# Kernel tuning notes

Measured on AMD Instinct MI355X. Metric: run time of the kernel, lower is better.

The kernel has to match this reference:

```python
import jax, jax.numpy as jnp
import numpy as np

B, D, K, H = 8192, 1024, 8, 2048


def setup_inputs() -> dict:
    key = jax.random.key(0)
    ks = jax.random.split(key, 4)
    x = jax.random.normal(ks[0], (B, D), dtype=jnp.float32)
    centroids = jax.random.normal(ks[1], (K, D), dtype=jnp.float32)
    W1 = jax.random.normal(ks[2], (K, D, H), dtype=jnp.float32) / np.sqrt(D).astype(np.float32)
    b1 = jnp.zeros((K, H), dtype=jnp.float32)
    W2 = jax.random.normal(ks[3], (K, H), dtype=jnp.float32) / np.sqrt(H).astype(np.float32)
    b2 = jnp.zeros((K,), dtype=jnp.float32)
    return {"x": x, "centroids": centroids, "W1": W1, "b1": b1, "W2": W2, "b2": b2}


def reference(x, centroids, W1, b1, W2, b2):
    # --- k-means hard routing: nearest centroid per sample (euclidean max_sim) ---
    # d2[b,k] = ||x_b||^2 - 2 x_b . c_k + ||c_k||^2  (avoid [B,K,D] blowup)
    d2 = (jnp.sum(x * x, axis=-1, keepdims=True)
          - 2.0 * (x @ centroids.T)
          + jnp.sum(centroids * centroids, axis=-1)[None, :])  # [B, K]
    cluster = jnp.argmin(d2, axis=-1)  # [B] int, hard assignment

    # --- per-expert log-likelihood heads (Einet stand-in), computed densely ---
    h = jnp.tanh(jnp.einsum("bd,kdh->kbh", x, W1) + b1[:, None, :])  # [K, B, H]
    lls = jnp.einsum("kbh,kh->kb", h, W2) + b2[:, None]              # [K, B]

    # --- combine: each sample takes the LL from its routed expert, original order ---
    lls_sorted = jnp.take_along_axis(lls.T, cluster[:, None], axis=1)[:, 0]  # [B]
    return lls_sorted
```

## Files before the change

kernel.cpp:

```cpp
#include <hip/hip_runtime.h>
#include <hip/hip_bf16.h>
#include <stdint.h>

#define B_N 8192
#define D_N 1024
#define K_N 8
#define H_N 2048

#define BM 320
#define BN 256
#define BK 64
#define GRID_MT 34
#define ABYTES 40960
#define BUFSZ 73728
#define RO_OFF 147456
#define PLL_OFF 148736
#define GEMM_LDS 153856

typedef unsigned int u32;
typedef unsigned short u16;
typedef __attribute__((ext_vector_type(8))) short short8;
typedef __attribute__((ext_vector_type(4))) float float4v;

struct __align__(8) us4 { u16 x, y, z, w; };

__device__ __forceinline__ u16 f2bf(float f) {
    union { float f; u32 u; } v; v.f = f;
    u32 u = v.u;
    u32 r = (u + 0x7fffu + ((u >> 16) & 1u)) >> 16;
    return (u16)r;
}

__device__ __forceinline__ float fast_tanh(float x) {
    float t = __expf(2.0f * x);
    return 1.0f - 2.0f * __builtin_amdgcn_rcpf(t + 1.0f);
}

__device__ __forceinline__ void async_copy16(void* lds, const void* g) {
    __builtin_amdgcn_global_load_lds(
        (const __attribute__((address_space(1))) void*)g,
        (__attribute__((address_space(3))) void*)lds, 16, 0, 0);
}

__global__ void route_kernel(const float* __restrict__ x,
                             const float* __restrict__ cent,
                             u16* __restrict__ xbf,
                             int* __restrict__ cluster,
                             u32* __restrict__ counts) {
    int tid = threadIdx.x;
    if (blockIdx.x == 0 && tid < K_N) counts[tid * 32] = 0;
    int wave = tid >> 6, lane = tid & 63;
    int b = blockIdx.x * 4 + wave;
    const float* xr = x + (size_t)b * D_N;

    float4 xv[4];
#pragma unroll
    for (int i = 0; i < 4; ++i)
        xv[i] = *(const float4*)(xr + i * 256 + lane * 4);

#pragma unroll
    for (int i = 0; i < 4; ++i) {
        us4 o;
        o.x = f2bf(xv[i].x); o.y = f2bf(xv[i].y);
        o.z = f2bf(xv[i].z); o.w = f2bf(xv[i].w);
        *(us4*)(xbf + (size_t)b * D_N + i * 256 + lane * 4) = o;
    }

    double acc[K_N];
#pragma unroll
    for (int k = 0; k < K_N; ++k) {
        const float* cr = cent + k * D_N;
        double s = 0.0;
#pragma unroll
        for (int i = 0; i < 4; ++i) {
            float4 cv = *(const float4*)(cr + i * 256 + lane * 4);
            double d0 = (double)xv[i].x - (double)cv.x; s += d0 * d0;
            double d1 = (double)xv[i].y - (double)cv.y; s += d1 * d1;
            double d2 = (double)xv[i].z - (double)cv.z; s += d2 * d2;
            double d3 = (double)xv[i].w - (double)cv.w; s += d3 * d3;
        }
        acc[k] = s;
    }
#pragma unroll
    for (int k = 0; k < K_N; ++k) {
        double v = acc[k];
        for (int off = 32; off; off >>= 1) v += __shfl_down(v, off);
        acc[k] = v;
    }
    if (lane == 0) {
        int best = 0; double bv = acc[0];
#pragma unroll
        for (int k = 1; k < K_N; ++k)
            if (acc[k] < bv) { bv = acc[k]; best = k; }
        cluster[b] = best;
    }
}

__global__ void scatter_kernel(const int* __restrict__ cluster,
                               u32* __restrict__ counts,
                               u32* __restrict__ idxl) {
    __shared__ u32 wcnt[4][K_N];
    __shared__ u32 gb[K_N];
    int tid = threadIdx.x;
    int b = blockIdx.x * 256 + tid;
    int lane = tid & 63, wid = tid >> 6;
    int cl = cluster[b];
    unsigned long long lower = (1ull << lane) - 1ull;
    u32 rank = 0;
#pragma unroll
    for (int k = 0; k < K_N; ++k) {
        unsigned long long mk = __ballot(cl == k);
        if (k == cl) rank = (u32)__popcll(mk & lower);
        if (lane == 0) wcnt[wid][k] = (u32)__popcll(mk);
    }
    __syncthreads();
    if (tid < K_N) {
        u32 tot = wcnt[0][tid] + wcnt[1][tid] + wcnt[2][tid] + wcnt[3][tid];
        gb[tid] = atomicAdd(&counts[tid * 32], tot);
    }
    __syncthreads();
    u32 woff = 0;
    if (wid > 0) woff += wcnt[0][cl];
    if (wid > 1) woff += wcnt[1][cl];
    if (wid > 2) woff += wcnt[2][cl];
    idxl[(size_t)cl * B_N + gb[cl] + woff + rank] = (u32)b;
}

__global__ void w1t_kernel(const float* __restrict__ w1, u16* __restrict__ w1t) {
    __shared__ float ts[64][65];
    int tid = threadIdx.x;
    int h0 = blockIdx.x * 64, d0 = blockIdx.y * 64, k = blockIdx.z;
    const float* src = w1 + ((size_t)k * D_N + d0) * H_N + h0;
#pragma unroll
    for (int i = 0; i < 4; ++i) {
        int q = i * 256 + tid;
        int r = q >> 4, c4 = (q & 15) * 4;
        float4 v = *(const float4*)(src + (size_t)r * H_N + c4);
        ts[c4 + 0][r] = v.x; ts[c4 + 1][r] = v.y;
        ts[c4 + 2][r] = v.z; ts[c4 + 3][r] = v.w;
    }
    __syncthreads();
    u16* dst = w1t + ((size_t)k * H_N + h0) * D_N + d0;
#pragma unroll
    for (int i = 0; i < 4; ++i) {
        int q = i * 256 + tid;
        int hr = q >> 4, d4 = (q & 15) * 4;
        us4 o;
        o.x = f2bf(ts[hr][d4 + 0]); o.y = f2bf(ts[hr][d4 + 1]);
        o.z = f2bf(ts[hr][d4 + 2]); o.w = f2bf(ts[hr][d4 + 3]);
        *(us4*)(dst + (size_t)hr * D_N + d4) = o;
    }
}

__global__ __launch_bounds__(512, 2) void gemm_kernel(
                            const u16* __restrict__ xbf,
                            const u16* __restrict__ w1t,
                            const float* __restrict__ b1,
                            const float* __restrict__ w2,
                            const u32* __restrict__ idxl,
                            const u32* __restrict__ counts,
                            float* __restrict__ llp) {
    extern __shared__ char lds[];
    int k = -1, mt = 0, ntile = 0;
#pragma unroll
    for (int kk = 0; kk < K_N; ++kk) {
        int c = (int)counts[kk * 32];
        int t = (c + BM - 1) / BM;
        if ((int)blockIdx.x >= ntile && (int)blockIdx.x < ntile + t) { k = kk; mt = (int)blockIdx.x - ntile; }
        ntile += t;
    }
    if (k < 0) return;
    int cnt = (int)counts[k * 32];
    int nc = blockIdx.y;
    int rows = cnt - mt * BM; if (rows > BM) rows = BM;
    int tid = threadIdx.x;
    int lane = tid & 63, w = tid >> 6;
    int wm = w >> 2, wn = w & 3;
    int wmbase = wm * 160;
    int h0 = nc * BN;
    int l15 = lane & 15, l4 = lane >> 4;

    u32* ro = (u32*)(lds + RO_OFF);
    float* pll = (float*)(lds + PLL_OFF);

    if (tid < BM) {
        int m = mt * BM + tid;
        int mm = m < cnt ? m : cnt - 1;
        ro[tid] = idxl[(size_t)k * B_N + mm] * (u32)(D_N * 2);
    }
    __syncthreads();

    u32 srcA[5], srcB[4];
#pragma unroll
    for (int i = 0; i < 5; ++i) {
        int c = i * 512 + tid; int r = c >> 3, j = c & 7;
        srcA[i] = ro[r] + ((u32)(j ^ (r & 7)) << 4);
    }
#pragma unroll
    for (int i = 0; i < 4; ++i) {
        int c = i * 512 + tid; int r = c >> 3, j = c & 7;
        srcB[i] = ((u32)(k * H_N + h0 + r) << 11) + ((u32)(j ^ (r & 7)) << 4);
    }
    const char* xb = (const char*)xbf;
    const char* wb = (const char*)w1t;

    int swz = l15 & 7;
    u32 aB0 = (u32)((wmbase + l15) * 128 + (((0 + l4) ^ swz) << 4));
    u32 aB1 = (u32)((wmbase + l15) * 128 + (((4 + l4) ^ swz) << 4));
    u32 bB0 = (u32)(ABYTES + (wn * 64 + l15) * 128 + (((0 + l4) ^ swz) << 4));
    u32 bB1 = (u32)(ABYTES + (wn * 64 + l15) * 128 + (((4 + l4) ^ swz) << 4));

    float4v acc[10][4];
#pragma unroll
    for (int mf = 0; mf < 10; ++mf)
#pragma unroll
        for (int nf = 0; nf < 4; ++nf)
            acc[mf][nf] = (float4v){0.f, 0.f, 0.f, 0.f};

#define STA(BUF, I, D) async_copy16((BUF) + (I) * 8192 + w * 1024, xb + srcA[I] + (D))
#define STB(BUF, I, D) async_copy16((BUF) + ABYTES + (I) * 8192 + w * 1024, wb + srcB[I] + (D))
#define BAR() do { asm volatile("" ::: "memory"); __builtin_amdgcn_s_barrier(); \
                   asm volatile("" ::: "memory"); } while (0)
#define LGKM0_PIN() do { asm volatile("s_waitcnt lgkmcnt(0)" ::: "memory"); \
                         __builtin_amdgcn_sched_barrier(0); } while (0)
#define MFMA_PHASE(MFB, BREG)                                                    \
    do {                                                                         \
        __builtin_amdgcn_s_setprio(1);                                           \
        _Pragma("unroll")                                                        \
        for (int i_ = 0; i_ < 5; ++i_) {                                         \
            if (wmbase + ((MFB) + i_) * 16 < rows) {                             \
                _Pragma("unroll")                                                \
                for (int nf_ = 0; nf_ < 4; ++nf_)                                \
                    acc[(MFB) + i_][nf_] = __builtin_amdgcn_mfma_f32_16x16x32_bf16( \
                        a[i_], BREG[nf_], acc[(MFB) + i_][nf_], 0, 0, 0);        \
            }                                                                    \
        }                                                                        \
        __builtin_amdgcn_s_setprio(0);                                           \
    } while (0)

    {
        char* Bp = lds;
        STA(Bp, 0, 0); STA(Bp, 1, 0); STA(Bp, 2, 0); STA(Bp, 3, 0); STA(Bp, 4, 0);
        STB(Bp, 0, 0); STB(Bp, 1, 0); STB(Bp, 2, 0); STB(Bp, 3, 0);
    }

    for (int t = 0; t < 16; ++t) {
        const char* Acur = lds + (t & 1) * BUFSZ;
        char* Bnx = lds + ((t + 1) & 1) * BUFSZ;
        u32 d = (u32)((t + 1) << 7);
        bool pre = (t < 15);
        short8 a[5], bC[4];

        asm volatile("s_waitcnt vmcnt(0)" ::: "memory");
        BAR();
#pragma unroll
        for (int nf = 0; nf < 4; ++nf)
            bC[nf] = *(const short8*)(Acur + bB0 + nf * 2048);
#pragma unroll
        for (int i = 0; i < 5; ++i)
            a[i] = *(const short8*)(Acur + aB0 + i * 2048);
        if (pre) { STB(Bnx, 0, d); STB(Bnx, 1, d); STB(Bnx, 2, d); }
        BAR();
        LGKM0_PIN();
        MFMA_PHASE(0, bC);

        BAR();
#pragma unroll
        for (int i = 0; i < 5; ++i)
            a[i] = *(const short8*)(Acur + aB0 + (5 + i) * 2048);
        if (pre) { STB(Bnx, 3, d); STA(Bnx, 0, d); STA(Bnx, 1, d); }
        BAR();
        LGKM0_PIN();
        MFMA_PHASE(5, bC);

        BAR();
#pragma unroll
        for (int nf = 0; nf < 4; ++nf)
            bC[nf] = *(const short8*)(Acur + bB1 + nf * 2048);
#pragma unroll
        for (int i = 0; i < 5; ++i)
            a[i] = *(const short8*)(Acur + aB1 + i * 2048);
        if (pre) { STA(Bnx, 2, d); STA(Bnx, 3, d); STA(Bnx, 4, d); }
        BAR();
        LGKM0_PIN();
        MFMA_PHASE(0, bC);

        BAR();
#pragma unroll
        for (int i = 0; i < 5; ++i)
            a[i] = *(const short8*)(Acur + aB1 + (5 + i) * 2048);
        BAR();
        LGKM0_PIN();
        MFMA_PHASE(5, bC);
    }

#undef STA
#undef STB
#undef BAR
#undef LGKM0_PIN
#undef MFMA_PHASE

    float w2v[4], b1v[4];
#pragma unroll
    for (int nf = 0; nf < 4; ++nf) {
        int h = h0 + wn * 64 + nf * 16 + l15;
        w2v[nf] = w2[k * H_N + h];
        b1v[nf] = b1[k * H_N + h];
    }
#pragma unroll
    for (int mf = 0; mf < 10; ++mf) {
        float rs[4] = {0.f, 0.f, 0.f, 0.f};
#pragma unroll
        for (int nf = 0; nf < 4; ++nf) {
#pragma unroll
            for (int r = 0; r < 4; ++r)
                rs[r] += fast_tanh(acc[mf][nf][r] + b1v[nf]) * w2v[nf];
        }
#pragma unroll
        for (int r = 0; r < 4; ++r) {
            float v = rs[r];
            v += __shfl_xor(v, 8);
            v += __shfl_xor(v, 4);
            v += __shfl_xor(v, 2);
            v += __shfl_xor(v, 1);
            if (l15 == 0) pll[wn * 320 + wmbase + mf * 16 + l4 * 4 + r] = v;
        }
    }
    __syncthreads();
    if (tid < BM) {
        int m = mt * BM + tid;
        if (m < cnt) {
            u32 b = idxl[(size_t)k * B_N + m];
            llp[(size_t)nc * B_N + b] = pll[tid] + pll[320 + tid] + pll[640 + tid] + pll[960 + tid];
        }
    }
}

__global__ void combine_kernel(const float* __restrict__ llp,
                               const int* __restrict__ cluster,
                               const float* __restrict__ b2,
                               float* __restrict__ out) {
    int b = blockIdx.x * 256 + threadIdx.x;
    float s = b2[cluster[b]];
#pragma unroll
    for (int nc = 0; nc < 8; ++nc) s += llp[(size_t)nc * B_N + b];
    out[b] = s;
}

extern "C" void kernel_launch(void* const* d_in, const int* in_sizes, int n_in,
                              void* d_out, int out_size, void* d_ws, size_t ws_size,
                              hipStream_t stream) {
    const float* x    = (const float*)d_in[0];
    const float* cent = (const float*)d_in[1];
    const float* W1   = (const float*)d_in[2];
    const float* b1   = (const float*)d_in[3];
    const float* W2   = (const float*)d_in[4];
    const float* b2   = (const float*)d_in[5];
    float* out = (float*)d_out;

    char* ws = (char*)d_ws;
    u16* xbf     = (u16*)(ws + 0);
    u16* w1t     = (u16*)(ws + 16777216);
    u32* counts  = (u32*)(ws + 50331648);
    int* cluster = (int*)(ws + 50332672);
    u32* idxl    = (u32*)(ws + 50365440);
    float* llp   = (float*)(ws + 50627584);

    (void)hipFuncSetAttribute((const void*)gemm_kernel,
                              hipFuncAttributeMaxDynamicSharedMemorySize, GEMM_LDS);

    hipLaunchKernelGGL(route_kernel, dim3(B_N / 4), dim3(256), 0, stream,
                       x, cent, xbf, cluster, counts);
    hipLaunchKernelGGL(scatter_kernel, dim3(32), dim3(256), 0, stream,
                       cluster, counts, idxl);
    hipLaunchKernelGGL(w1t_kernel, dim3(H_N / 64, D_N / 64, K_N), dim3(256), 0, stream,
                       W1, w1t);
    hipLaunchKernelGGL(gemm_kernel, dim3(GRID_MT, 8), dim3(512), GEMM_LDS, stream,
                       xbf, w1t, b1, W2, idxl, counts, llp);
    hipLaunchKernelGGL(combine_kernel, dim3(B_N / 256), dim3(256), 0, stream,
                       llp, cluster, b2, out);
}
```

Before: 87.06 us.

## Fold scatter into routing via atomics and swap GEMM grid axes

Measured after the change: 151.0 us. 1.73x slower.

```diff
diff --git a/kernel.cpp b/kernel.cpp
--- a/kernel.cpp
+++ b/kernel.cpp
@@ -42,13 +42,42 @@
         (__attribute__((address_space(3))) void*)lds, 16, 0, 0);
 }
 
+__global__ void w1t_kernel(const float* __restrict__ w1, u16* __restrict__ w1t,
+                           u32* __restrict__ counts) {
+    __shared__ float ts[64][65];
+    int tid = threadIdx.x;
+    if (blockIdx.x == 0 && blockIdx.y == 0 && blockIdx.z == 0 && tid < K_N)
+        counts[tid * 32] = 0;
+    int h0 = blockIdx.x * 64, d0 = blockIdx.y * 64, k = blockIdx.z;
+    const float* src = w1 + ((size_t)k * D_N + d0) * H_N + h0;
+#pragma unroll
+    for (int i = 0; i < 4; ++i) {
+        int q = i * 256 + tid;
+        int r = q >> 4, c4 = (q & 15) * 4;
+        float4 v = *(const float4*)(src + (size_t)r * H_N + c4);
+        ts[c4 + 0][r] = v.x; ts[c4 + 1][r] = v.y;
+        ts[c4 + 2][r] = v.z; ts[c4 + 3][r] = v.w;
+    }
+    __syncthreads();
+    u16* dst = w1t + ((size_t)k * H_N + h0) * D_N + d0;
+#pragma unroll
+    for (int i = 0; i < 4; ++i) {
+        int q = i * 256 + tid;
+        int hr = q >> 4, d4 = (q & 15) * 4;
+        us4 o;
+        o.x = f2bf(ts[hr][d4 + 0]); o.y = f2bf(ts[hr][d4 + 1]);
+        o.z = f2bf(ts[hr][d4 + 2]); o.w = f2bf(ts[hr][d4 + 3]);
+        *(us4*)(dst + (size_t)hr * D_N + d4) = o;
+    }
+}
+
 __global__ void route_kernel(const float* __restrict__ x,
                              const float* __restrict__ cent,
                              u16* __restrict__ xbf,
                              int* __restrict__ cluster,
-                             u32* __restrict__ counts) {
+                             u32* __restrict__ counts,
+                             u32* __restrict__ idxl) {
     int tid = threadIdx.x;
-    if (blockIdx.x == 0 && tid < K_N) counts[tid * 32] = 0;
     int wave = tid >> 6, lane = tid & 63;
     int b = blockIdx.x * 4 + wave;
     const float* xr = x + (size_t)b * D_N;
@@ -93,62 +122,8 @@
         for (int k = 1; k < K_N; ++k)
             if (acc[k] < bv) { bv = acc[k]; best = k; }
         cluster[b] = best;
-    }
-}
-
-__global__ void scatter_kernel(const int* __restrict__ cluster,
-                               u32* __restrict__ counts,
-                               u32* __restrict__ idxl) {
-    __shared__ u32 wcnt[4][K_N];
-    __shared__ u32 gb[K_N];
-    int tid = threadIdx.x;
-    int b = blockIdx.x * 256 + tid;
-    int lane = tid & 63, wid = tid >> 6;
-    int cl = cluster[b];
-    unsigned long long lower = (1ull << lane) - 1ull;
-    u32 rank = 0;
-#pragma unroll
-    for (int k = 0; k < K_N; ++k) {
-        unsigned long long mk = __ballot(cl == k);
-        if (k == cl) rank = (u32)__popcll(mk & lower);
-        if (lane == 0) wcnt[wid][k] = (u32)__popcll(mk);
-    }
-    __syncthreads();
-    if (tid < K_N) {
-        u32 tot = wcnt[0][tid] + wcnt[1][tid] + wcnt[2][tid] + wcnt[3][tid];
-        gb[tid] = atomicAdd(&counts[tid * 32], tot);
-    }
-    __syncthreads();
-    u32 woff = 0;
-    if (wid > 0) woff += wcnt[0][cl];
-    if (wid > 1) woff += wcnt[1][cl];
-    if (wid > 2) woff += wcnt[2][cl];
-    idxl[(size_t)cl * B_N + gb[cl] + woff + rank] = (u32)b;
-}
-
-__global__ void w1t_kernel(const float* __restrict__ w1, u16* __restrict__ w1t) {
-    __shared__ float ts[64][65];
-    int tid = threadIdx.x;
-    int h0 = blockIdx.x * 64, d0 = blockIdx.y * 64, k = blockIdx.z;
-    const float* src = w1 + ((size_t)k * D_N + d0) * H_N + h0;
-#pragma unroll
-    for (int i = 0; i < 4; ++i) {
-        int q = i * 256 + tid;
-        int r = q >> 4, c4 = (q & 15) * 4;
-        float4 v = *(const float4*)(src + (size_t)r * H_N + c4);
-        ts[c4 + 0][r] = v.x; ts[c4 + 1][r] = v.y;
-        ts[c4 + 2][r] = v.z; ts[c4 + 3][r] = v.w;
-    }
-    __syncthreads();
-    u16* dst = w1t + ((size_t)k * H_N + h0) * D_N + d0;
-#pragma unroll
-    for (int i = 0; i < 4; ++i) {
-        int q = i * 256 + tid;
-        int hr = q >> 4, d4 = (q & 15) * 4;
-        us4 o;
-        o.x = f2bf(ts[hr][d4 + 0]); o.y = f2bf(ts[hr][d4 + 1]);
-        o.z = f2bf(ts[hr][d4 + 2]); o.w = f2bf(ts[hr][d4 + 3]);
-        *(us4*)(dst + (size_t)hr * D_N + d4) = o;
+        u32 r = atomicAdd(&counts[best * 32], 1u);
+        idxl[(size_t)best * B_N + r] = (u32)b;
     }
 }
 
@@ -161,17 +136,18 @@
                             const u32* __restrict__ counts,
                             float* __restrict__ llp) {
     extern __shared__ char lds[];
+    int tix = (int)blockIdx.y;
     int k = -1, mt = 0, ntile = 0;
 #pragma unroll
     for (int kk = 0; kk < K_N; ++kk) {
         int c = (int)counts[kk * 32];
         int t = (c + BM - 1) / BM;
-        if ((int)blockIdx.x >= ntile && (int)blockIdx.x < ntile + t) { k = kk; mt = (int)blockIdx.x - ntile; }
+        if (tix >= ntile && tix < ntile + t) { k = kk; mt = tix - ntile; }
         ntile += t;
     }
     if (k < 0) return;
     int cnt = (int)counts[k * 32];
-    int nc = blockIdx.y;
+    int nc = (int)blockIdx.x;
     int rows = cnt - mt * BM; if (rows > BM) rows = BM;
     int tid = threadIdx.x;
     int lane = tid & 63, w = tid >> 6;
@@ -369,13 +345,11 @@
     (void)hipFuncSetAttribute((const void*)gemm_kernel,
                               hipFuncAttributeMaxDynamicSharedMemorySize, GEMM_LDS);
 
+    hipLaunchKernelGGL(w1t_kernel, dim3(H_N / 64, D_N / 64, K_N), dim3(256), 0, stream,
+                       W1, w1t, counts);
     hipLaunchKernelGGL(route_kernel, dim3(B_N / 4), dim3(256), 0, stream,
-                       x, cent, xbf, cluster, counts);
-    hipLaunchKernelGGL(scatter_kernel, dim3(32), dim3(256), 0, stream,
-                       cluster, counts, idxl);
-    hipLaunchKernelGGL(w1t_kernel, dim3(H_N / 64, D_N / 64, K_N), dim3(256), 0, stream,
-                       W1, w1t);
-    hipLaunchKernelGGL(gemm_kernel, dim3(GRID_MT, 8), dim3(512), GEMM_LDS, stream,
+                       x, cent, xbf, cluster, counts, idxl);
+    hipLaunchKernelGGL(gemm_kernel, dim3(8, GRID_MT), dim3(512), GEMM_LDS, stream,
                        xbf, w1t, b1, W2, idxl, counts, llp);
     hipLaunchKernelGGL(combine_kernel, dim3(B_N / 256), dim3(256), 0, stream,
                        llp, cluster, b2, out);
```

## Fuse combine into GEMM via atomics and swap grid axes for N-chunk locality

Applied to the files above, without the earlier changes.

Measured after the change: 85.66 us. Within noise of the previous version (-1.6%).

```diff
diff --git a/kernel.cpp b/kernel.cpp
--- a/kernel.cpp
+++ b/kernel.cpp
@@ -42,13 +42,42 @@
         (__attribute__((address_space(3))) void*)lds, 16, 0, 0);
 }
 
+__global__ void w1t_kernel(const float* __restrict__ w1, u16* __restrict__ w1t,
+                           u32* __restrict__ counts) {
+    __shared__ float ts[64][65];
+    int tid = threadIdx.x;
+    if (blockIdx.x == 0 && blockIdx.y == 0 && blockIdx.z == 0 && tid < K_N)
+        counts[tid * 32] = 0;
+    int h0 = blockIdx.x * 64, d0 = blockIdx.y * 64, k = blockIdx.z;
+    const float* src = w1 + ((size_t)k * D_N + d0) * H_N + h0;
+#pragma unroll
+    for (int i = 0; i < 4; ++i) {
+        int q = i * 256 + tid;
+        int r = q >> 4, c4 = (q & 15) * 4;
+        float4 v = *(const float4*)(src + (size_t)r * H_N + c4);
+        ts[c4 + 0][r] = v.x; ts[c4 + 1][r] = v.y;
+        ts[c4 + 2][r] = v.z; ts[c4 + 3][r] = v.w;
+    }
+    __syncthreads();
+    u16* dst = w1t + ((size_t)k * H_N + h0) * D_N + d0;
+#pragma unroll
+    for (int i = 0; i < 4; ++i) {
+        int q = i * 256 + tid;
+        int hr = q >> 4, d4 = (q & 15) * 4;
+        us4 o;
+        o.x = f2bf(ts[hr][d4 + 0]); o.y = f2bf(ts[hr][d4 + 1]);
+        o.z = f2bf(ts[hr][d4 + 2]); o.w = f2bf(ts[hr][d4 + 3]);
+        *(us4*)(dst + (size_t)hr * D_N + d4) = o;
+    }
+}
+
 __global__ void route_kernel(const float* __restrict__ x,
                              const float* __restrict__ cent,
+                             const float* __restrict__ b2,
                              u16* __restrict__ xbf,
                              int* __restrict__ cluster,
-                             u32* __restrict__ counts) {
+                             float* __restrict__ out) {
     int tid = threadIdx.x;
-    if (blockIdx.x == 0 && tid < K_N) counts[tid * 32] = 0;
     int wave = tid >> 6, lane = tid & 63;
     int b = blockIdx.x * 4 + wave;
     const float* xr = x + (size_t)b * D_N;
@@ -93,6 +122,7 @@
         for (int k = 1; k < K_N; ++k)
             if (acc[k] < bv) { bv = acc[k]; best = k; }
         cluster[b] = best;
+        out[b] = b2[best];
     }
 }
 
@@ -126,32 +156,6 @@
     idxl[(size_t)cl * B_N + gb[cl] + woff + rank] = (u32)b;
 }
 
-__global__ void w1t_kernel(const float* __restrict__ w1, u16* __restrict__ w1t) {
-    __shared__ float ts[64][65];
-    int tid = threadIdx.x;
-    int h0 = blockIdx.x * 64, d0 = blockIdx.y * 64, k = blockIdx.z;
-    const float* src = w1 + ((size_t)k * D_N + d0) * H_N + h0;
-#pragma unroll
-    for (int i = 0; i < 4; ++i) {
-        int q = i * 256 + tid;
-        int r = q >> 4, c4 = (q & 15) * 4;
-        float4 v = *(const float4*)(src + (size_t)r * H_N + c4);
-        ts[c4 + 0][r] = v.x; ts[c4 + 1][r] = v.y;
-        ts[c4 + 2][r] = v.z; ts[c4 + 3][r] = v.w;
-    }
-    __syncthreads();
-    u16* dst = w1t + ((size_t)k * H_N + h0) * D_N + d0;
-#pragma unroll
-    for (int i = 0; i < 4; ++i) {
-        int q = i * 256 + tid;
-        int hr = q >> 4, d4 = (q & 15) * 4;
-        us4 o;
-        o.x = f2bf(ts[hr][d4 + 0]); o.y = f2bf(ts[hr][d4 + 1]);
-        o.z = f2bf(ts[hr][d4 + 2]); o.w = f2bf(ts[hr][d4 + 3]);
-        *(us4*)(dst + (size_t)hr * D_N + d4) = o;
-    }
-}
-
 __global__ __launch_bounds__(512, 2) void gemm_kernel(
                             const u16* __restrict__ xbf,
                             const u16* __restrict__ w1t,
@@ -159,19 +163,20 @@
                             const float* __restrict__ w2,
                             const u32* __restrict__ idxl,
                             const u32* __restrict__ counts,
-                            float* __restrict__ llp) {
+                            float* __restrict__ out) {
     extern __shared__ char lds[];
+    int tix = (int)blockIdx.y;
     int k = -1, mt = 0, ntile = 0;
 #pragma unroll
     for (int kk = 0; kk < K_N; ++kk) {
         int c = (int)counts[kk * 32];
         int t = (c + BM - 1) / BM;
-        if ((int)blockIdx.x >= ntile && (int)blockIdx.x < ntile + t) { k = kk; mt = (int)blockIdx.x - ntile; }
+        if (tix >= ntile && tix < ntile + t) { k = kk; mt = tix - ntile; }
         ntile += t;
     }
     if (k < 0) return;
     int cnt = (int)counts[k * 32];
-    int nc = blockIdx.y;
+    int nc = (int)blockIdx.x;
     int rows = cnt - mt * BM; if (rows > BM) rows = BM;
     int tid = threadIdx.x;
     int lane = tid & 63, w = tid >> 6;
@@ -331,20 +336,9 @@
         int m = mt * BM + tid;
         if (m < cnt) {
             u32 b = idxl[(size_t)k * B_N + m];
-            llp[(size_t)nc * B_N + b] = pll[tid] + pll[320 + tid] + pll[640 + tid] + pll[960 + tid];
+            atomicAdd(&out[b], pll[tid] + pll[320 + tid] + pll[640 + tid] + pll[960 + tid]);
         }
     }
-}
-
-__global__ void combine_kernel(const float* __restrict__ llp,
-                               const int* __restrict__ cluster,
-                               const float* __restrict__ b2,
-                               float* __restrict__ out) {
-    int b = blockIdx.x * 256 + threadIdx.x;
-    float s = b2[cluster[b]];
-#pragma unroll
-    for (int nc = 0; nc < 8; ++nc) s += llp[(size_t)nc * B_N + b];
-    out[b] = s;
 }
 
 extern "C" void kernel_launch(void* const* d_in, const int* in_sizes, int n_in,
@@ -364,19 +358,16 @@
     u32* counts  = (u32*)(ws + 50331648);
     int* cluster = (int*)(ws + 50332672);
     u32* idxl    = (u32*)(ws + 50365440);
-    float* llp   = (float*)(ws + 50627584);
 
     (void)hipFuncSetAttribute((const void*)gemm_kernel,
                               hipFuncAttributeMaxDynamicSharedMemorySize, GEMM_LDS);
 
+    hipLaunchKernelGGL(w1t_kernel, dim3(H_N / 64, D_N / 64, K_N), dim3(256), 0, stream,
+                       W1, w1t, counts);
     hipLaunchKernelGGL(route_kernel, dim3(B_N / 4), dim3(256), 0, stream,
-                       x, cent, xbf, cluster, counts);
+                       x, cent, b2, xbf, cluster, out);
     hipLaunchKernelGGL(scatter_kernel, dim3(32), dim3(256), 0, stream,
                        cluster, counts, idxl);
-    hipLaunchKernelGGL(w1t_kernel, dim3(H_N / 64, D_N / 64, K_N), dim3(256), 0, stream,
-                       W1, w1t);
-    hipLaunchKernelGGL(gemm_kernel, dim3(GRID_MT, 8), dim3(512), GEMM_LDS, stream,
-                       xbf, w1t, b1, W2, idxl, counts, llp);
-    hipLaunchKernelGGL(combine_kernel, dim3(B_N / 256), dim3(256), 0, stream,
-                       llp, cluster, b2, out);
-}
+    hipLaunchKernelGGL(gemm_kernel, dim3(8, GRID_MT), dim3(512), GEMM_LDS, stream,
+                       xbf, w1t, b1, W2, idxl, counts, out);
+}
```
